# Optimization experiments

Measured on AMD Instinct MI355X. Metric: run time of the kernel, lower is better.

Reference implementation:

```python
import jax, jax.numpy as jnp
from jax import lax
import numpy as np


def _layernorm(x, g, b, eps=1e-5):
    m = x.mean(-1, keepdims=True)
    v = ((x - m) ** 2).mean(-1, keepdims=True)
    return (x - m) / jnp.sqrt(v + eps) * g + b


def _selective_ssm(x, Wxz, convw, convb, Wdt, bdt, Alog, Dp, WB, WC):
    # x: [B, T, D]. Mamba-style selective scan.
    Bsz, T, D = x.shape
    dconv = convw.shape[-1]
    xz = x @ Wxz.T                      # [B,T,2D]
    x_ssm = xz[..., :D]
    # depthwise causal conv: torch pads both sides (dconv-1) then keeps [:T] == left-pad only
    xc = lax.conv_general_dilated(
        x_ssm.transpose(0, 2, 1), convw, window_strides=(1,),
        padding=[(dconv - 1, 0)], dimension_numbers=("NCH", "OIH", "NCH"),
        feature_group_count=D) + convb[None, :, None]
    xc = jax.nn.silu(xc.transpose(0, 2, 1))          # [B,T,D]
    dt = jax.nn.softplus(xc @ Wdt.T + bdt)           # [B,T,D]
    A = -jnp.exp(Alog)                               # [D,N]
    Bm = xc @ WB.T                                   # [B,T,N]
    Cm = xc @ WC.T                                   # [B,T,N]

    def step(h, inp):
        dt_t, B_t, C_t, x_t = inp                    # [B,D],[B,N],[B,N],[B,D]
        dA = jnp.exp(A[None] * dt_t[:, :, None])     # [B,D,N]
        h = h * dA + x_t[:, :, None] * (dt_t[:, :, None] * B_t[:, None, :])
        y = jnp.einsum("bdn,bn->bd", h, C_t)
        return h, y

    h0 = jnp.zeros((Bsz, D, A.shape[1]), x.dtype)
    _, ys = lax.scan(step, h0, (dt.transpose(1, 0, 2), Bm.transpose(1, 0, 2),
                                Cm.transpose(1, 0, 2), x.transpose(1, 0, 2)))
    return ys.transpose(1, 0, 2) + x * Dp[None, None, :]


def reference(emb, first_pass, W_in, b_in, ln_in_g, ln_in_b, site_tab, hour_tab,
              W_meta, b_meta, pos_enc, fwd_Wxz, fwd_convw, fwd_convb, fwd_Wdt,
              fwd_bdt, fwd_Alog, fwd_D, fwd_WB, fwd_WC, bwd_Wxz, bwd_convw,
              bwd_convb, bwd_Wdt, bwd_bdt, bwd_Alog, bwd_D, bwd_WB, bwd_WC,
              W_merge, b_merge, ln_g, ln_b, W_out, b_out, site_ids, hours):
    T = emb.shape[1]
    x = jnp.concatenate([emb, first_pass], -1)
    h = jax.nn.gelu(_layernorm(x @ W_in.T + b_in, ln_in_g, ln_in_b),
                    approximate=False) + pos_enc[:, :T]
    meta_in = jnp.concatenate([site_tab[jnp.clip(site_ids, 0, site_tab.shape[0] - 1)],
                               hour_tab[jnp.clip(hours, 0, 23)]], -1)
    h = h + (meta_in @ W_meta.T + b_meta)[:, None, :]
    res = h
    h_f = _selective_ssm(h, fwd_Wxz, fwd_convw, fwd_convb, fwd_Wdt, fwd_bdt,
                         fwd_Alog, fwd_D, fwd_WB, fwd_WC)
    h_b = jnp.flip(_selective_ssm(jnp.flip(h, 1), bwd_Wxz, bwd_convw, bwd_convb,
                                  bwd_Wdt, bwd_bdt, bwd_Alog, bwd_D, bwd_WB,
                                  bwd_WC), 1)
    h = jnp.concatenate([h_f, h_b], -1) @ W_merge.T + b_merge  # dropout = eval no-op
    h = _layernorm(h + res, ln_g, ln_b)
    return h @ W_out.T + b_out


def setup_inputs() -> dict:
    D, N, Din, Ds, T, B, M, C, dconv = 64, 8, 1536, 234, 12, 4096, 8, 234, 4
    keys = iter(jax.random.split(jax.random.key(0), 64))

    def rn(shape, s=0.1):
        return jax.random.normal(next(keys), shape, jnp.float32) * s

    def ssm(pfx):
        return {
            pfx + "_Wxz": rn((2 * D, D)), pfx + "_convw": rn((D, 1, dconv), 0.3),
            pfx + "_convb": rn((D,), 0.02), pfx + "_Wdt": rn((D, D)),
            pfx + "_bdt": rn((D,), 0.02),
            pfx + "_Alog": jnp.log(jnp.tile(jnp.arange(1, N + 1, dtype=jnp.float32)[None, :], (D, 1))),
            pfx + "_D": jnp.ones((D,), jnp.float32),
            pfx + "_WB": rn((N, D)), pfx + "_WC": rn((N, D)),
        }

    inp = {
        "emb": jax.random.normal(next(keys), (B, T, Din), jnp.float32),
        "first_pass": jax.random.uniform(next(keys), (B, T, Ds), jnp.float32),
        "W_in": rn((D, Din + Ds), 0.02), "b_in": jnp.zeros((D,), jnp.float32),
        "ln_in_g": jnp.ones((D,), jnp.float32), "ln_in_b": jnp.zeros((D,), jnp.float32),
        "site_tab": rn((20, M), 1.0), "hour_tab": rn((24, M), 1.0),
        "W_meta": rn((D, 2 * M)), "b_meta": jnp.zeros((D,), jnp.float32),
        "pos_enc": rn((1, T, D), 0.02),
        "W_merge": rn((D, 2 * D)), "b_merge": jnp.zeros((D,), jnp.float32),
        "ln_g": jnp.ones((D,), jnp.float32), "ln_b": jnp.zeros((D,), jnp.float32),
        "W_out": rn((C, D), 0.02), "b_out": jnp.zeros((C,), jnp.float32),
        "site_ids": jax.random.randint(next(keys), (B,), 0, 20),
        "hours": jax.random.randint(next(keys), (B,), 0, 24),
    }
    inp.update(ssm("fwd"))
    inp.update(ssm("bwd"))
    return inp
```

## Files before the change

kernel.cpp:

```cpp
#include <hip/hip_runtime.h>

typedef unsigned short u16;
typedef unsigned int u32;
typedef __attribute__((ext_vector_type(8))) short short8;
typedef __attribute__((ext_vector_type(4))) float fx4;

#define BATCH 4096
#define TSEQ 12
#define DIN 1536
#define DS 234
#define KTOT 1770
#define KPAD 1792
#define COUT 234
#define MROWS (BATCH * TSEQ)

union F4 { float4 v; float f[4]; u32 u[4]; };
union ABFrag { u32 u[4]; short8 s; uint4 q4; };

__device__ __attribute__((aligned(256))) u16 gWhi[64 * KPAD];
__device__ __attribute__((aligned(256))) u16 gWlo[64 * KPAD];
__device__ __attribute__((aligned(256))) float gH[(size_t)MROWS * 64];

__device__ __forceinline__ void splitPair(float x0, float x1, u32& hi, u32& lo) {
    union { float f; u32 u; } c0, c1, l0, l1;
    union { u32 u; float f; } g0, g1;
    c0.f = x0; c1.f = x1;
    u32 h0 = c0.u & 0xFFFF0000u;
    u32 h1 = c1.u & 0xFFFF0000u;
    g0.u = h0; g1.u = h1;
    l0.f = x0 - g0.f;
    l1.f = x1 - g1.f;
    hi = (h0 >> 16) | h1;
    lo = (l0.u >> 16) | (l1.u & 0xFFFF0000u);
}

__device__ __forceinline__ void splitFrag(const float a[8], ABFrag& ah, ABFrag& al) {
#pragma unroll
    for (int i = 0; i < 4; i++) splitPair(a[2 * i], a[2 * i + 1], ah.u[i], al.u[i]);
}

__device__ __forceinline__ void loadRow(F4 (&w)[16], const float* base) {
#pragma unroll
    for (int i = 0; i < 16; i++) w[i].v = *(const float4*)(base + 4 * i);
}
__device__ __forceinline__ float dot64(const F4 (&w)[16], const float* v) {
    float a = 0.f, b = 0.f;
#pragma unroll
    for (int i = 0; i < 16; i++) {
        F4 h; h.v = *(const float4*)(v + 4 * i);
        a += w[i].f[0] * h.f[0] + w[i].f[1] * h.f[1];
        b += w[i].f[2] * h.f[2] + w[i].f[3] * h.f[3];
    }
    return a + b;
}

__global__ __launch_bounds__(256) void k_wsplit(const float* __restrict__ W_in) {
    int idx = blockIdx.x * 256 + threadIdx.x;
    int n = idx / KPAD, k = idx - n * KPAD;
    float w = (k < KTOT) ? W_in[n * KTOT + k] : 0.f;
    union { float f; u32 u; } c; c.f = w;
    u32 h = c.u & 0xFFFF0000u;
    union { u32 u; float f; } g; g.u = h;
    union { float f; u32 u; } l; l.f = w - g.f;
    gWhi[idx] = (u16)(h >> 16);
    gWlo[idx] = (u16)(l.u >> 16);
}

__global__ __launch_bounds__(64) void k_gemm(
    const float* __restrict__ emb, const float* __restrict__ fpass,
    const float* __restrict__ b_in, const float* __restrict__ ln_in_g,
    const float* __restrict__ ln_in_b)
{
    const int lane = threadIdx.x;
    const int q = lane >> 4, cc = lane & 15;
    const int ko = q * 8;
    const int rowblk = blockIdx.x * 64;

    fx4 acc[4][4];
#pragma unroll
    for (int tl = 0; tl < 4; tl++)
#pragma unroll
        for (int nt = 0; nt < 4; nt++) acc[tl][nt] = (fx4){0.f, 0.f, 0.f, 0.f};

    const float* arows[4];
    const float* frows[4];
#pragma unroll
    for (int tl = 0; tl < 4; tl++) {
        size_t m = (size_t)(rowblk + tl * 16 + cc);
        arows[tl] = emb + m * DIN + ko;
        frows[tl] = fpass + m * DS + ko;
    }
    const u16* whb = gWhi + cc * KPAD + ko;
    const u16* wlb = gWlo + cc * KPAD + ko;

    for (int kg = 0; kg < DIN; kg += 32) {
        ABFrag bh[4], bl[4];
#pragma unroll
        for (int nt = 0; nt < 4; nt++) {
            bh[nt].q4 = *(const uint4*)(whb + nt * 16 * KPAD + kg);
            bl[nt].q4 = *(const uint4*)(wlb + nt * 16 * KPAD + kg);
        }
#pragma unroll
        for (int tl = 0; tl < 4; tl++) {
            F4 a0, a1;
            a0.v = *(const float4*)(arows[tl] + kg);
            a1.v = *(const float4*)(arows[tl] + kg + 4);
            float av[8] = {a0.f[0], a0.f[1], a0.f[2], a0.f[3], a1.f[0], a1.f[1], a1.f[2], a1.f[3]};
            ABFrag ah, al;
            splitFrag(av, ah, al);
#pragma unroll
            for (int nt = 0; nt < 4; nt++) {
                acc[tl][nt] = __builtin_amdgcn_mfma_f32_16x16x32_bf16(ah.s, bh[nt].s, acc[tl][nt], 0, 0, 0);
                acc[tl][nt] = __builtin_amdgcn_mfma_f32_16x16x32_bf16(al.s, bh[nt].s, acc[tl][nt], 0, 0, 0);
                acc[tl][nt] = __builtin_amdgcn_mfma_f32_16x16x32_bf16(ah.s, bl[nt].s, acc[tl][nt], 0, 0, 0);
            }
        }
    }
    for (int kg = 0; kg < 224; kg += 32) {
        ABFrag bh[4], bl[4];
#pragma unroll
        for (int nt = 0; nt < 4; nt++) {
            bh[nt].q4 = *(const uint4*)(whb + nt * 16 * KPAD + DIN + kg);
            bl[nt].q4 = *(const uint4*)(wlb + nt * 16 * KPAD + DIN + kg);
        }
#pragma unroll
        for (int tl = 0; tl < 4; tl++) {
            float2 a0 = *(const float2*)(frows[tl] + kg);
            float2 a1 = *(const float2*)(frows[tl] + kg + 2);
            float2 a2 = *(const float2*)(frows[tl] + kg + 4);
            float2 a3 = *(const float2*)(frows[tl] + kg + 6);
            float av[8] = {a0.x, a0.y, a1.x, a1.y, a2.x, a2.y, a3.x, a3.y};
            ABFrag ah, al;
            splitFrag(av, ah, al);
#pragma unroll
            for (int nt = 0; nt < 4; nt++) {
                acc[tl][nt] = __builtin_amdgcn_mfma_f32_16x16x32_bf16(ah.s, bh[nt].s, acc[tl][nt], 0, 0, 0);
                acc[tl][nt] = __builtin_amdgcn_mfma_f32_16x16x32_bf16(al.s, bh[nt].s, acc[tl][nt], 0, 0, 0);
                acc[tl][nt] = __builtin_amdgcn_mfma_f32_16x16x32_bf16(ah.s, bl[nt].s, acc[tl][nt], 0, 0, 0);
            }
        }
    }
    {
        ABFrag bh[4], bl[4];
#pragma unroll
        for (int nt = 0; nt < 4; nt++) {
            bh[nt].q4 = *(const uint4*)(whb + nt * 16 * KPAD + DIN + 224);
            bl[nt].q4 = *(const uint4*)(wlb + nt * 16 * KPAD + DIN + 224);
        }
#pragma unroll
        for (int tl = 0; tl < 4; tl++) {
            float av[8];
#pragma unroll
            for (int j = 0; j < 8; j++) {
                int kk = 224 + ko + j;
                av[j] = (kk < DS) ? frows[tl][224 + j] : 0.f;
            }
            ABFrag ah, al;
            splitFrag(av, ah, al);
#pragma unroll
            for (int nt = 0; nt < 4; nt++) {
                acc[tl][nt] = __builtin_amdgcn_mfma_f32_16x16x32_bf16(ah.s, bh[nt].s, acc[tl][nt], 0, 0, 0);
                acc[tl][nt] = __builtin_amdgcn_mfma_f32_16x16x32_bf16(al.s, bh[nt].s, acc[tl][nt], 0, 0, 0);
                acc[tl][nt] = __builtin_amdgcn_mfma_f32_16x16x32_bf16(ah.s, bl[nt].s, acc[tl][nt], 0, 0, 0);
            }
        }
    }
    float bia[4], gg[4], bb2[4];
#pragma unroll
    for (int nt = 0; nt < 4; nt++) {
        int col = nt * 16 + cc;
        bia[nt] = b_in[col]; gg[nt] = ln_in_g[col]; bb2[nt] = ln_in_b[col];
    }
#pragma unroll
    for (int tl = 0; tl < 4; tl++) {
#pragma unroll
        for (int rr = 0; rr < 4; rr++) {
            float vv[4], s1 = 0.f, s2 = 0.f;
#pragma unroll
            for (int nt = 0; nt < 4; nt++) {
                vv[nt] = acc[tl][nt][rr] + bia[nt];
                s1 += vv[nt]; s2 += vv[nt] * vv[nt];
            }
#pragma unroll
            for (int off = 1; off <= 8; off <<= 1) {
                s1 += __shfl_xor(s1, off);
                s2 += __shfl_xor(s2, off);
            }
            float mean = s1 * 0.015625f;
            float var = s2 * 0.015625f - mean * mean;
            float rstd = rsqrtf(var + 1e-5f);
            size_t m = (size_t)(rowblk + tl * 16 + q * 4 + rr);
#pragma unroll
            for (int nt = 0; nt < 4; nt++) {
                float x = (vv[nt] - mean) * rstd * gg[nt] + bb2[nt];
                float gel = 0.5f * x * (1.f + erff(x * 0.70710678118654752f));
                gH[m * 64 + nt * 16 + cc] = gel;
            }
        }
    }
}

__global__ __launch_bounds__(64) void k_ssm(
    const float* __restrict__ site_tab, const float* __restrict__ hour_tab,
    const float* __restrict__ W_meta, const float* __restrict__ b_meta,
    const float* __restrict__ pos_enc,
    const float* __restrict__ Wm, const float* __restrict__ bm,
    const float* __restrict__ lng, const float* __restrict__ lnb,
    const float* __restrict__ Wo, const float* __restrict__ bo,
    const int* __restrict__ site_ids, const int* __restrict__ hours,
    const float* __restrict__ fWxz, const float* __restrict__ fconvw, const float* __restrict__ fconvb,
    const float* __restrict__ fWdt, const float* __restrict__ fbdt, const float* __restrict__ fAlog,
    const float* __restrict__ fDp, const float* __restrict__ fWB, const float* __restrict__ fWC,
    const float* __restrict__ bWxz, const float* __restrict__ bconvw, const float* __restrict__ bconvb,
    const float* __restrict__ bWdt, const float* __restrict__ bbdt, const float* __restrict__ bAlog,
    const float* __restrict__ bDp, const float* __restrict__ bWB, const float* __restrict__ bWC,
    float* __restrict__ out)
{
    __shared__ __attribute__((aligned(16))) float Hs[TSEQ * 64];
    __shared__ __attribute__((aligned(16))) float Xs[TSEQ * 64];
    __shared__ __attribute__((aligned(16))) float BCs[TSEQ * 16];
    __shared__ __attribute__((aligned(16))) float Ys[TSEQ * 128];

    const int lane = threadIdx.x;
    const int b = blockIdx.x;

    float metaV;
    {
        int sid = min(max(site_ids[b], 0), 19);
        int hr  = min(max(hours[b], 0), 23);
        float a = b_meta[lane];
#pragma unroll
        for (int j = 0; j < 8; j++) a += site_tab[sid * 8 + j] * W_meta[lane * 16 + j];
#pragma unroll
        for (int j = 0; j < 8; j++) a += hour_tab[hr * 8 + j] * W_meta[lane * 16 + 8 + j];
        metaV = a;
    }
#pragma unroll
    for (int t = 0; t < TSEQ; t++)
        Hs[t * 64 + lane] = gH[((size_t)b * TSEQ + t) * 64 + lane] + pos_enc[t * 64 + lane] + metaV;
    __syncthreads();

#pragma unroll 1
    for (int dir = 0; dir < 2; dir++) {
        const float* Wxz  = dir ? bWxz  : fWxz;
        const float* cw   = dir ? bconvw : fconvw;
        const float* cbp  = dir ? bconvb : fconvb;
        const float* Wdt  = dir ? bWdt  : fWdt;
        const float* bdt  = dir ? bbdt  : fbdt;
        const float* Alog = dir ? bAlog : fAlog;
        const float* Dp   = dir ? bDp   : fDp;
        const float* WB   = dir ? bWB   : fWB;
        const float* WC   = dir ? bWC   : fWC;

        float xs[TSEQ];
        {
            F4 rw[16]; loadRow(rw, Wxz + lane * 64);
#pragma unroll
            for (int s = 0; s < TSEQ; s++) {
                int t = dir ? (TSEQ - 1 - s) : s;
                xs[s] = dot64(rw, Hs + t * 64);
            }
        }
        {
            float w0 = cw[lane * 4 + 0], w1 = cw[lane * 4 + 1];
            float w2 = cw[lane * 4 + 2], w3 = cw[lane * 4 + 3];
            float cb = cbp[lane];
#pragma unroll
            for (int s = 0; s < TSEQ; s++) {
                float a = cb + w3 * xs[s];
                if (s >= 1) a += w2 * xs[s - 1];
                if (s >= 2) a += w1 * xs[s - 2];
                if (s >= 3) a += w0 * xs[s - 3];
                float sig = 1.f / (1.f + __expf(-a));
                Xs[s * 64 + lane] = a * sig;
            }
        }
        __syncthreads();

        float dtv[TSEQ];
        {
            F4 rw[16]; loadRow(rw, Wdt + lane * 64);
            float bdv = bdt[lane];
#pragma unroll
            for (int s = 0; s < TSEQ; s++) {
                float a = bdv + dot64(rw, Xs + s * 64);
                dtv[s] = fmaxf(a, 0.f) + log1pf(__expf(-fabsf(a)));
            }
        }
        {
            const int n = lane & 7, s1 = lane >> 3;
#pragma unroll 1
            for (int sel = 0; sel < 2; sel++) {
                F4 rw[16]; loadRow(rw, (sel ? WC : WB) + n * 64);
                BCs[s1 * 16 + sel * 8 + n] = dot64(rw, Xs + s1 * 64);
                if (lane < 32)
                    BCs[(8 + s1) * 16 + sel * 8 + n] = dot64(rw, Xs + (8 + s1) * 64);
            }
        }
        __syncthreads();

        {
            float An[8];
#pragma unroll
            for (int n2 = 0; n2 < 8; n2++) An[n2] = -__expf(Alog[lane * 8 + n2]);
            float dpv = Dp[lane];
            float st[8] = {0.f, 0.f, 0.f, 0.f, 0.f, 0.f, 0.f, 0.f};
#pragma unroll
            for (int s = 0; s < TSEQ; s++) {
                int t = dir ? (TSEQ - 1 - s) : s;
                float dtc = dtv[s];
                float xv = Hs[t * 64 + lane];
                float coef = xv * dtc;
                const float* bcp = BCs + s * 16;
                float y = 0.f;
#pragma unroll
                for (int n2 = 0; n2 < 8; n2++) {
                    float dA = __expf(An[n2] * dtc);
                    st[n2] = st[n2] * dA + coef * bcp[n2];
                    y += st[n2] * bcp[8 + n2];
                }
                Ys[t * 128 + (dir << 6) + lane] = y + xv * dpv;
            }
        }
        __syncthreads();
    }

    {
        float mv[TSEQ];
        float bmv = bm[lane];
#pragma unroll
        for (int t = 0; t < TSEQ; t++) mv[t] = bmv + Hs[t * 64 + lane];
#pragma unroll 1
        for (int half = 0; half < 2; half++) {
            F4 rw[16]; loadRow(rw, Wm + lane * 128 + half * 64);
#pragma unroll
            for (int t = 0; t < TSEQ; t++) mv[t] += dot64(rw, Ys + t * 128 + half * 64);
        }
        float g = lng[lane], be = lnb[lane];
#pragma unroll
        for (int t = 0; t < TSEQ; t++) {
            float v = mv[t];
            float s1 = v, s2 = v * v;
#pragma unroll
            for (int off = 1; off <= 32; off <<= 1) {
                s1 += __shfl_xor(s1, off);
                s2 += __shfl_xor(s2, off);
            }
            float mean = s1 * 0.015625f;
            float var = s2 * 0.015625f - mean * mean;
            float rs = rsqrtf(var + 1e-5f);
            Xs[t * 64 + lane] = (v - mean) * rs * g + be;
        }
    }
    __syncthreads();

#pragma unroll 1
    for (int ci = 0; ci < 4; ci++) {
        int cidx = ci * 64 + lane;
        bool act = cidx < COUT;
        F4 rw[16];
        float bov = 0.f;
        if (act) { loadRow(rw, Wo + (size_t)cidx * 64); bov = bo[cidx]; }
        for (int t = 0; t < TSEQ; t++) {
            if (act) {
                float a = bov + dot64(rw, Xs + t * 64);
                out[((size_t)b * TSEQ + t) * COUT + cidx] = a;
            }
        }
    }
}

extern "C" void kernel_launch(void* const* d_in, const int* in_sizes, int n_in,
                              void* d_out, int out_size, void* d_ws, size_t ws_size,
                              hipStream_t stream) {
    (void)d_ws; (void)ws_size; (void)in_sizes; (void)n_in; (void)out_size;

    k_wsplit<<<(64 * KPAD) / 256, 256, 0, stream>>>((const float*)d_in[2]);

    k_gemm<<<MROWS / 64, 64, 0, stream>>>(
        (const float*)d_in[0], (const float*)d_in[1],
        (const float*)d_in[3], (const float*)d_in[4], (const float*)d_in[5]);

    k_ssm<<<BATCH, 64, 0, stream>>>(
        (const float*)d_in[6], (const float*)d_in[7], (const float*)d_in[8], (const float*)d_in[9],
        (const float*)d_in[10],
        (const float*)d_in[11], (const float*)d_in[12], (const float*)d_in[13], (const float*)d_in[14],
        (const float*)d_in[15], (const float*)d_in[16],
        (const int*)d_in[17], (const int*)d_in[18],
        (const float*)d_in[19], (const float*)d_in[20], (const float*)d_in[21], (const float*)d_in[22],
        (const float*)d_in[23], (const float*)d_in[24], (const float*)d_in[25], (const float*)d_in[26],
        (const float*)d_in[27],
        (const float*)d_in[28], (const float*)d_in[29], (const float*)d_in[30], (const float*)d_in[31],
        (const float*)d_in[32], (const float*)d_in[33], (const float*)d_in[34], (const float*)d_in[35],
        (const float*)d_in[36],
        (float*)d_out);
}
```

Measured before the change: 1.307 ms.

## Split SSM directions across two wavefronts and halve GEMM row tile

The SSM kernel now launches 128 threads per batch element so the forward and backward scans run on separate wavefronts at the same time. The merge and output projections are also split across both waves, with per-wave padded shared buffers and a separate merge buffer. The input GEMM tile drops from 64 to 32 rows per block, doubling the grid, and both kernels get occupancy hints, aiming at more parallelism and latency hiding. The trade-off is that each GEMM block reuses its weight fragments over half as many rows, so weight traffic per row goes up.

```diff
diff --git a/kernel.cpp b/kernel.cpp
--- a/kernel.cpp
+++ b/kernel.cpp
@@ -66,7 +66,7 @@
     gWlo[idx] = (u16)(l.u >> 16);
 }
 
-__global__ __launch_bounds__(64) void k_gemm(
+__global__ __launch_bounds__(64, 3) void k_gemm(
     const float* __restrict__ emb, const float* __restrict__ fpass,
     const float* __restrict__ b_in, const float* __restrict__ ln_in_g,
     const float* __restrict__ ln_in_b)
@@ -74,18 +74,18 @@
     const int lane = threadIdx.x;
     const int q = lane >> 4, cc = lane & 15;
     const int ko = q * 8;
-    const int rowblk = blockIdx.x * 64;
-
-    fx4 acc[4][4];
-#pragma unroll
-    for (int tl = 0; tl < 4; tl++)
+    const int rowblk = blockIdx.x * 32;
+
+    fx4 acc[2][4];
+#pragma unroll
+    for (int tl = 0; tl < 2; tl++)
 #pragma unroll
         for (int nt = 0; nt < 4; nt++) acc[tl][nt] = (fx4){0.f, 0.f, 0.f, 0.f};
 
-    const float* arows[4];
-    const float* frows[4];
-#pragma unroll
-    for (int tl = 0; tl < 4; tl++) {
+    const float* arows[2];
+    const float* frows[2];
+#pragma unroll
+    for (int tl = 0; tl < 2; tl++) {
         size_t m = (size_t)(rowblk + tl * 16 + cc);
         arows[tl] = emb + m * DIN + ko;
         frows[tl] = fpass + m * DS + ko;
@@ -101,7 +101,7 @@
             bl[nt].q4 = *(const uint4*)(wlb + nt * 16 * KPAD + kg);
         }
 #pragma unroll
-        for (int tl = 0; tl < 4; tl++) {
+        for (int tl = 0; tl < 2; tl++) {
             F4 a0, a1;
             a0.v = *(const float4*)(arows[tl] + kg);
             a1.v = *(const float4*)(arows[tl] + kg + 4);
@@ -124,7 +124,7 @@
             bl[nt].q4 = *(const uint4*)(wlb + nt * 16 * KPAD + DIN + kg);
         }
 #pragma unroll
-        for (int tl = 0; tl < 4; tl++) {
+        for (int tl = 0; tl < 2; tl++) {
             float2 a0 = *(const float2*)(frows[tl] + kg);
             float2 a1 = *(const float2*)(frows[tl] + kg + 2);
             float2 a2 = *(const float2*)(frows[tl] + kg + 4);
@@ -148,7 +148,7 @@
             bl[nt].q4 = *(const uint4*)(wlb + nt * 16 * KPAD + DIN + 224);
         }
 #pragma unroll
-        for (int tl = 0; tl < 4; tl++) {
+        for (int tl = 0; tl < 2; tl++) {
             float av[8];
 #pragma unroll
             for (int j = 0; j < 8; j++) {
@@ -172,7 +172,7 @@
         bia[nt] = b_in[col]; gg[nt] = ln_in_g[col]; bb2[nt] = ln_in_b[col];
     }
 #pragma unroll
-    for (int tl = 0; tl < 4; tl++) {
+    for (int tl = 0; tl < 2; tl++) {
 #pragma unroll
         for (int rr = 0; rr < 4; rr++) {
             float vv[4], s1 = 0.f, s2 = 0.f;
@@ -200,7 +200,7 @@
     }
 }
 
-__global__ __launch_bounds__(64) void k_ssm(
+__global__ __launch_bounds__(128, 3) void k_ssm(
     const float* __restrict__ site_tab, const float* __restrict__ hour_tab,
     const float* __restrict__ W_meta, const float* __restrict__ b_meta,
     const float* __restrict__ pos_enc,
@@ -217,11 +217,13 @@
     float* __restrict__ out)
 {
     __shared__ __attribute__((aligned(16))) float Hs[TSEQ * 64];
-    __shared__ __attribute__((aligned(16))) float Xs[TSEQ * 64];
-    __shared__ __attribute__((aligned(16))) float BCs[TSEQ * 16];
+    __shared__ __attribute__((aligned(16))) float Xs[2][TSEQ * 68];
+    __shared__ __attribute__((aligned(16))) float BCs[2][TSEQ * 16];
     __shared__ __attribute__((aligned(16))) float Ys[TSEQ * 128];
-
-    const int lane = threadIdx.x;
+    __shared__ __attribute__((aligned(16))) float Ms[TSEQ * 64];
+
+    const int lane = threadIdx.x & 63;
+    const int w = threadIdx.x >> 6;
     const int b = blockIdx.x;
 
     float metaV;
@@ -236,12 +238,14 @@
         metaV = a;
     }
 #pragma unroll
-    for (int t = 0; t < TSEQ; t++)
+    for (int tt = 0; tt < 6; tt++) {
+        int t = w * 6 + tt;
         Hs[t * 64 + lane] = gH[((size_t)b * TSEQ + t) * 64 + lane] + pos_enc[t * 64 + lane] + metaV;
+    }
     __syncthreads();
 
-#pragma unroll 1
-    for (int dir = 0; dir < 2; dir++) {
+    {
+        const int dir = w;
         const float* Wxz  = dir ? bWxz  : fWxz;
         const float* cw   = dir ? bconvw : fconvw;
         const float* cbp  = dir ? bconvb : fconvb;
@@ -251,6 +255,8 @@
         const float* Dp   = dir ? bDp   : fDp;
         const float* WB   = dir ? bWB   : fWB;
         const float* WC   = dir ? bWC   : fWC;
+        float* Xd = Xs[w];
+        float* BCd = BCs[w];
 
         float xs[TSEQ];
         {
@@ -272,7 +278,7 @@
                 if (s >= 2) a += w1 * xs[s - 2];
                 if (s >= 3) a += w0 * xs[s - 3];
                 float sig = 1.f / (1.f + __expf(-a));
-                Xs[s * 64 + lane] = a * sig;
+                Xd[s * 68 + lane] = a * sig;
             }
         }
         __syncthreads();
@@ -283,7 +289,7 @@
             float bdv = bdt[lane];
 #pragma unroll
             for (int s = 0; s < TSEQ; s++) {
-                float a = bdv + dot64(rw, Xs + s * 64);
+                float a = bdv + dot64(rw, Xd + s * 68);
                 dtv[s] = fmaxf(a, 0.f) + log1pf(__expf(-fabsf(a)));
             }
         }
@@ -292,9 +298,9 @@
 #pragma unroll 1
             for (int sel = 0; sel < 2; sel++) {
                 F4 rw[16]; loadRow(rw, (sel ? WC : WB) + n * 64);
-                BCs[s1 * 16 + sel * 8 + n] = dot64(rw, Xs + s1 * 64);
+                BCd[s1 * 16 + sel * 8 + n] = dot64(rw, Xd + s1 * 68);
                 if (lane < 32)
-                    BCs[(8 + s1) * 16 + sel * 8 + n] = dot64(rw, Xs + (8 + s1) * 64);
+                    BCd[(8 + s1) * 16 + sel * 8 + n] = dot64(rw, Xd + (8 + s1) * 68);
             }
         }
         __syncthreads();
@@ -311,7 +317,7 @@
                 float dtc = dtv[s];
                 float xv = Hs[t * 64 + lane];
                 float coef = xv * dtc;
-                const float* bcp = BCs + s * 16;
+                const float* bcp = BCd + s * 16;
                 float y = 0.f;
 #pragma unroll
                 for (int n2 = 0; n2 < 8; n2++) {
@@ -326,20 +332,21 @@
     }
 
     {
-        float mv[TSEQ];
+        float mv[6];
         float bmv = bm[lane];
 #pragma unroll
-        for (int t = 0; t < TSEQ; t++) mv[t] = bmv + Hs[t * 64 + lane];
+        for (int tt = 0; tt < 6; tt++) mv[tt] = bmv + Hs[(w * 6 + tt) * 64 + lane];
 #pragma unroll 1
         for (int half = 0; half < 2; half++) {
             F4 rw[16]; loadRow(rw, Wm + lane * 128 + half * 64);
 #pragma unroll
-            for (int t = 0; t < TSEQ; t++) mv[t] += dot64(rw, Ys + t * 128 + half * 64);
+            for (int tt = 0; tt < 6; tt++)
+                mv[tt] += dot64(rw, Ys + (w * 6 + tt) * 128 + half * 64);
         }
         float g = lng[lane], be = lnb[lane];
 #pragma unroll
-        for (int t = 0; t < TSEQ; t++) {
-            float v = mv[t];
+        for (int tt = 0; tt < 6; tt++) {
+            float v = mv[tt];
             float s1 = v, s2 = v * v;
 #pragma unroll
             for (int off = 1; off <= 32; off <<= 1) {
@@ -349,21 +356,21 @@
             float mean = s1 * 0.015625f;
             float var = s2 * 0.015625f - mean * mean;
             float rs = rsqrtf(var + 1e-5f);
-            Xs[t * 64 + lane] = (v - mean) * rs * g + be;
+            Ms[(w * 6 + tt) * 64 + lane] = (v - mean) * rs * g + be;
         }
     }
     __syncthreads();
 
 #pragma unroll 1
-    for (int ci = 0; ci < 4; ci++) {
-        int cidx = ci * 64 + lane;
+    for (int ci2 = 0; ci2 < 2; ci2++) {
+        int cidx = (w * 2 + ci2) * 64 + lane;
         bool act = cidx < COUT;
         F4 rw[16];
         float bov = 0.f;
         if (act) { loadRow(rw, Wo + (size_t)cidx * 64); bov = bo[cidx]; }
         for (int t = 0; t < TSEQ; t++) {
             if (act) {
-                float a = bov + dot64(rw, Xs + t * 64);
+                float a = bov + dot64(rw, Ms + t * 64);
                 out[((size_t)b * TSEQ + t) * COUT + cidx] = a;
             }
         }
@@ -377,11 +384,11 @@
 
     k_wsplit<<<(64 * KPAD) / 256, 256, 0, stream>>>((const float*)d_in[2]);
 
-    k_gemm<<<MROWS / 64, 64, 0, stream>>>(
+    k_gemm<<<MROWS / 32, 64, 0, stream>>>(
         (const float*)d_in[0], (const float*)d_in[1],
         (const float*)d_in[3], (const float*)d_in[4], (const float*)d_in[5]);
 
-    k_ssm<<<BATCH, 64, 0, stream>>>(
+    k_ssm<<<BATCH, 128, 0, stream>>>(
         (const float*)d_in[6], (const float*)d_in[7], (const float*)d_in[8], (const float*)d_in[9],
         (const float*)d_in[10],
         (const float*)d_in[11], (const float*)d_in[12], (const float*)d_in[13], (const float*)d_in[14],
```

New measurement: 2.685 ms. 2.05x slower.
